# Kernel optimization log

Hardware: AMD Instinct MI355X
Metric: run time of the kernel (lower is better)

Reference implementation:

```python
import jax, jax.numpy as jnp
import numpy as np

D_MODEL, HEAD_DIM = 1024, 128

def setup_inputs() -> dict:
    key = jax.random.key(0)
    kx, kq, kk, kv = jax.random.split(key, 4)
    x = jax.random.normal(kx, (4, 4096, D_MODEL), dtype=jnp.float32)
    s = 1.0 / np.sqrt(D_MODEL)
    Wq = jax.random.normal(kq, (D_MODEL, HEAD_DIM), dtype=jnp.float32) * s
    Wk = jax.random.normal(kk, (D_MODEL, HEAD_DIM), dtype=jnp.float32) * s
    Wv = jax.random.normal(kv, (D_MODEL, HEAD_DIM), dtype=jnp.float32) * s
    return {"x": x, "Wq": Wq, "Wk": Wk, "Wv": Wv}

def reference(x, Wq, Wk, Wv):
    # x: [b, s, d_model]; Wq/Wk/Wv: [d_model, head_dim]
    q = jnp.einsum('bsd,dh->bsh', x, Wq)
    k = jnp.einsum('bsd,dh->bsh', x, Wk)
    v = jnp.einsum('bsd,dh->bsh', x, Wv)
    seq = x.shape[1]
    scale = 1.0 / jnp.sqrt(jnp.asarray(q.shape[-1], q.dtype))
    scores = jnp.einsum('bqh,bkh->bqk', q, k) * scale  # [b, s, s]
    causal = jnp.tril(jnp.ones((seq, seq), dtype=bool))
    scores = jnp.where(causal, scores, jnp.asarray(-jnp.inf, scores.dtype))
    attn = jax.nn.softmax(scores, axis=-1)
    return jnp.einsum('bqk,bkh->bqh', attn, v)
```

## Files before the change

### kernel.cpp

```cpp
#include <hip/hip_runtime.h>
#include <hip/hip_bf16.h>
#include <math.h>

#define D_MODEL 1024
#define HD 128
#define SEQ 4096

typedef __bf16 bf16x8 __attribute__((ext_vector_type(8)));
typedef float f32x4 __attribute__((ext_vector_type(4)));
typedef unsigned int u32;
typedef u32 u32x4 __attribute__((ext_vector_type(4)));

__device__ __forceinline__ unsigned short f2bf(float f) {
    union { float f; u32 u; } c; c.f = f;
    u32 u = c.u;
    u = (u + 0x7fffu + ((u >> 16) & 1u)) >> 16;
    return (unsigned short)u;
}
__device__ __forceinline__ u32 pk2(float a, float b) {
    __hip_bfloat162 h = __float22bfloat162_rn(make_float2(a, b));
    union { __hip_bfloat162 h; u32 u; } c; c.h = h; return c.u;
}

__global__ __launch_bounds__(256)
void wt_kernel(const float* __restrict__ Wq, const float* __restrict__ Wk,
               const float* __restrict__ Wv, unsigned short* __restrict__ Wt) {
    __shared__ float wsf[64][129];
    const int t = threadIdx.x;
    const int k0 = blockIdx.x * 64;
    const int mat = blockIdx.y;
    const float* W = (mat == 0) ? Wq : (mat == 1) ? Wk : Wv;
    const float sc = (mat == 0) ? (0.08838834764831845f * 1.4426950408889634f) : 1.0f;
    {
        const int r = t >> 2, c = (t & 3) * 32;
        const float* src = W + (size_t)(k0 + r) * HD + c;
        #pragma unroll
        for (int j = 0; j < 32; j += 4)
            *reinterpret_cast<f32x4*>(&wsf[r][c + j]) = *reinterpret_cast<const f32x4*>(src + j);
    }
    __syncthreads();
    const int n = t >> 1, ks = (t & 1) * 32;
    u32 ow[16];
    #pragma unroll
    for (int j = 0; j < 16; ++j)
        ow[j] = pk2(wsf[ks + 2 * j][n] * sc, wsf[ks + 2 * j + 1][n] * sc);
    unsigned short* dst = Wt + (size_t)(mat * HD + n) * D_MODEL + k0 + ks;
    #pragma unroll
    for (int j = 0; j < 4; ++j)
        *reinterpret_cast<u32x4*>(dst + j * 8) = (u32x4){ow[4*j], ow[4*j+1], ow[4*j+2], ow[4*j+3]};
}

__global__ __launch_bounds__(256)
void proj_kernel(const float* __restrict__ x, const unsigned short* __restrict__ Wt,
                 unsigned short* __restrict__ Qb, unsigned short* __restrict__ Kb,
                 unsigned short* __restrict__ Vt) {
    __shared__ __align__(16) unsigned short xs[64][72];
    __shared__ __align__(16) unsigned short wts[128][72];
    const int t = threadIdx.x;
    const int w = t >> 6, lane = t & 63, li = lane & 15, g2 = lane >> 4;
    const int nbase = blockIdx.x * 128;
    const int rowbase = blockIdx.y * 64;
    const int xr = t >> 2, xc = (t & 3) * 16;
    const int wr = t >> 1, wc = (t & 1) * 32;

    f32x4 acc[8];
    #pragma unroll
    for (int nt = 0; nt < 8; ++nt) acc[nt] = (f32x4){0.f, 0.f, 0.f, 0.f};

    f32x4 xv[4];
    bf16x8 wv[4];
    {
        const float* xp = x + (size_t)(rowbase + xr) * D_MODEL + xc;
        #pragma unroll
        for (int j = 0; j < 4; ++j) xv[j] = *reinterpret_cast<const f32x4*>(xp + j * 4);
        const unsigned short* wp = Wt + (size_t)(nbase + wr) * D_MODEL + wc;
        #pragma unroll
        for (int j = 0; j < 4; ++j) wv[j] = *reinterpret_cast<const bf16x8*>(wp + j * 8);
    }

    for (int k0 = 0; k0 < D_MODEL; k0 += 64) {
        union { u32 d[8]; bf16x8 v[2]; } cv;
        cv.d[0] = pk2(xv[0][0], xv[0][1]); cv.d[1] = pk2(xv[0][2], xv[0][3]);
        cv.d[2] = pk2(xv[1][0], xv[1][1]); cv.d[3] = pk2(xv[1][2], xv[1][3]);
        cv.d[4] = pk2(xv[2][0], xv[2][1]); cv.d[5] = pk2(xv[2][2], xv[2][3]);
        cv.d[6] = pk2(xv[3][0], xv[3][1]); cv.d[7] = pk2(xv[3][2], xv[3][3]);
        *reinterpret_cast<bf16x8*>(&xs[xr][xc])     = cv.v[0];
        *reinterpret_cast<bf16x8*>(&xs[xr][xc + 8]) = cv.v[1];
        #pragma unroll
        for (int j = 0; j < 4; ++j)
            *reinterpret_cast<bf16x8*>(&wts[wr][wc + j * 8]) = wv[j];
        __syncthreads();
        if (k0 + 64 < D_MODEL) {
            const float* xp = x + (size_t)(rowbase + xr) * D_MODEL + (k0 + 64) + xc;
            #pragma unroll
            for (int j = 0; j < 4; ++j) xv[j] = *reinterpret_cast<const f32x4*>(xp + j * 4);
            const unsigned short* wp = Wt + (size_t)(nbase + wr) * D_MODEL + (k0 + 64) + wc;
            #pragma unroll
            for (int j = 0; j < 4; ++j) wv[j] = *reinterpret_cast<const bf16x8*>(wp + j * 8);
        }
        #pragma unroll
        for (int kk = 0; kk < 2; ++kk) {
            bf16x8 af = *reinterpret_cast<const bf16x8*>(&xs[w * 16 + li][kk * 32 + g2 * 8]);
            #pragma unroll
            for (int nt = 0; nt < 8; ++nt) {
                bf16x8 bfr = *reinterpret_cast<const bf16x8*>(&wts[nt * 16 + li][kk * 32 + g2 * 8]);
                acc[nt] = __builtin_amdgcn_mfma_f32_16x16x32_bf16(af, bfr, acc[nt], 0, 0, 0);
            }
        }
        __syncthreads();
    }

    if (nbase < 256) {
        unsigned short* P = nbase ? Kb : Qb;
        #pragma unroll
        for (int nt = 0; nt < 8; ++nt)
            #pragma unroll
            for (int r = 0; r < 4; ++r) {
                int grow = rowbase + w * 16 + g2 * 4 + r;
                P[(size_t)grow * HD + nt * 16 + li] = f2bf(acc[nt][r]);
            }
    } else {
        int grow0 = rowbase + w * 16 + g2 * 4;
        int b_ = grow0 >> 12, s_ = grow0 & 4095;
        #pragma unroll
        for (int nt = 0; nt < 8; ++nt) {
            ushort4 s4;
            s4.x = f2bf(acc[nt][0]); s4.y = f2bf(acc[nt][1]);
            s4.z = f2bf(acc[nt][2]); s4.w = f2bf(acc[nt][3]);
            *reinterpret_cast<ushort4*>(&Vt[((size_t)b_ * HD + nt * 16 + li) * SEQ + s_]) = s4;
        }
    }
}

__global__ __launch_bounds__(256, 2)
void attn_kernel(const unsigned short* __restrict__ Qb, const unsigned short* __restrict__ Kb,
                 const unsigned short* __restrict__ Vt, float* __restrict__ outO,
                 unsigned short* __restrict__ Obf, float* __restrict__ Lbuf) {
    __shared__ __align__(16) char smem[46080];
    unsigned short (*Klds)[136] = (unsigned short(*)[136])(smem);
    unsigned short (*Vlds)[72]  = (unsigned short(*)[72])(smem + 17408);
    const int t = threadIdx.x;
    const int w = t >> 6, lane = t & 63, li = lane & 15, g2 = lane >> 4;
    const int qh = w >> 1, kh = w & 1;
    unsigned short (*Pw)[40] = (unsigned short(*)[40])(smem + 35840 + w * 2560);

    const int b = blockIdx.x & 3;
    const int u = blockIdx.x >> 2;
    const int g = 63 - (u >> 2);
    const int c = u & 3;
    const int R = g + 1;
    const int ts = (c * R) >> 2, te = ((c + 1) * R) >> 2;
    const int q0 = g * 64;
    const size_t rowb = (size_t)b * SEQ;
    const int koff = kh * 32;

    const int kr = t >> 2, kc = (t & 3) * 32;
    const int vr = t >> 1, vc = (t & 1) * 32;

    bf16x8 qf[2][4];
    #pragma unroll
    for (int qt = 0; qt < 2; ++qt)
        #pragma unroll
        for (int ks = 0; ks < 4; ++ks)
            qf[qt][ks] = *reinterpret_cast<const bf16x8*>(
                Qb + (rowb + q0 + qh * 32 + qt * 16 + li) * HD + ks * 32 + g2 * 8);

    f32x4 acco[2][8];
    #pragma unroll
    for (int qt = 0; qt < 2; ++qt)
        #pragma unroll
        for (int dt = 0; dt < 8; ++dt) acco[qt][dt] = (f32x4){0.f, 0.f, 0.f, 0.f};
    float ls[2][4] = {{0.f,0.f,0.f,0.f},{0.f,0.f,0.f,0.f}};

    bf16x8 kv_[4], vv_[4];
    if (ts < te) {
        const unsigned short* kp = Kb + (rowb + (size_t)ts * 64 + kr) * HD + kc;
        const unsigned short* vp = Vt + ((size_t)b * HD + vr) * SEQ + (size_t)ts * 64 + vc;
        #pragma unroll
        for (int j = 0; j < 4; ++j) kv_[j] = *reinterpret_cast<const bf16x8*>(kp + j * 8);
        #pragma unroll
        for (int j = 0; j < 4; ++j) vv_[j] = *reinterpret_cast<const bf16x8*>(vp + j * 8);
    }

    for (int it = ts; it < te; ++it) {
        #pragma unroll
        for (int j = 0; j < 4; ++j)
            *reinterpret_cast<bf16x8*>(&Klds[kr][kc + j * 8]) = kv_[j];
        #pragma unroll
        for (int j = 0; j < 4; ++j)
            *reinterpret_cast<bf16x8*>(&Vlds[vr][vc + j * 8]) = vv_[j];
        __syncthreads();
        if (it + 1 < te) {
            const unsigned short* kp = Kb + (rowb + (size_t)(it + 1) * 64 + kr) * HD + kc;
            const unsigned short* vp = Vt + ((size_t)b * HD + vr) * SEQ + (size_t)(it + 1) * 64 + vc;
            #pragma unroll
            for (int j = 0; j < 4; ++j) kv_[j] = *reinterpret_cast<const bf16x8*>(kp + j * 8);
            #pragma unroll
            for (int j = 0; j < 4; ++j) vv_[j] = *reinterpret_cast<const bf16x8*>(vp + j * 8);
        }

        f32x4 accs[2][2];
        #pragma unroll
        for (int qt = 0; qt < 2; ++qt)
            #pragma unroll
            for (int kt = 0; kt < 2; ++kt) accs[qt][kt] = (f32x4){0.f, 0.f, 0.f, 0.f};
        #pragma unroll
        for (int kt = 0; kt < 2; ++kt)
            #pragma unroll
            for (int ks = 0; ks < 4; ++ks) {
                bf16x8 kf = *reinterpret_cast<const bf16x8*>(&Klds[koff + kt * 16 + li][ks * 32 + g2 * 8]);
                accs[0][kt] = __builtin_amdgcn_mfma_f32_16x16x32_bf16(qf[0][ks], kf, accs[0][kt], 0, 0, 0);
                accs[1][kt] = __builtin_amdgcn_mfma_f32_16x16x32_bf16(qf[1][ks], kf, accs[1][kt], 0, 0, 0);
            }

        const bool masked = (it == g);
        float p[2][2][4];
        #pragma unroll
        for (int qt = 0; qt < 2; ++qt)
            #pragma unroll
            for (int kt = 0; kt < 2; ++kt)
                #pragma unroll
                for (int r = 0; r < 4; ++r) {
                    float s = accs[qt][kt][r];
                    if (masked && (koff + kt * 16 + li > qh * 32 + qt * 16 + g2 * 4 + r))
                        s = -INFINITY;
                    p[qt][kt][r] = __builtin_amdgcn_exp2f(s - 16.0f);
                }
        #pragma unroll
        for (int qt = 0; qt < 2; ++qt)
            #pragma unroll
            for (int r = 0; r < 4; ++r)
                ls[qt][r] += p[qt][0][r] + p[qt][1][r];

        #pragma unroll
        for (int qt = 0; qt < 2; ++qt)
            #pragma unroll
            for (int kt = 0; kt < 2; ++kt)
                #pragma unroll
                for (int r = 0; r < 4; ++r)
                    Pw[qt * 16 + g2 * 4 + r][kt * 16 + li] = f2bf(p[qt][kt][r]);
        bf16x8 pf0 = *reinterpret_cast<const bf16x8*>(&Pw[li][g2 * 8]);
        bf16x8 pf1 = *reinterpret_cast<const bf16x8*>(&Pw[16 + li][g2 * 8]);

        #pragma unroll
        for (int dt = 0; dt < 8; ++dt) {
            bf16x8 vf = *reinterpret_cast<const bf16x8*>(&Vlds[dt * 16 + li][koff + g2 * 8]);
            acco[0][dt] = __builtin_amdgcn_mfma_f32_16x16x32_bf16(pf0, vf, acco[0][dt], 0, 0, 0);
            acco[1][dt] = __builtin_amdgcn_mfma_f32_16x16x32_bf16(pf1, vf, acco[1][dt], 0, 0, 0);
        }
        __syncthreads();
    }

    #pragma unroll
    for (int d = 1; d < 16; d <<= 1)
        #pragma unroll
        for (int qt = 0; qt < 2; ++qt)
            #pragma unroll
            for (int r = 0; r < 4; ++r)
                ls[qt][r] += __shfl_xor(ls[qt][r], d);

    float (*Osum)[132] = (float(*)[132])smem;
    float* Lsh = (float*)(smem + 33792);
    __syncthreads();
    if (kh == 0) {
        #pragma unroll
        for (int qt = 0; qt < 2; ++qt) {
            #pragma unroll
            for (int dt = 0; dt < 8; ++dt)
                #pragma unroll
                for (int r = 0; r < 4; ++r)
                    Osum[qh * 32 + qt * 16 + g2 * 4 + r][dt * 16 + li] = acco[qt][dt][r];
            if (li == 0)
                #pragma unroll
                for (int r = 0; r < 4; ++r)
                    Lsh[qh * 32 + qt * 16 + g2 * 4 + r] = ls[qt][r];
        }
    }
    __syncthreads();
    if (kh == 1) {
        #pragma unroll
        for (int qt = 0; qt < 2; ++qt) {
            #pragma unroll
            for (int dt = 0; dt < 8; ++dt)
                #pragma unroll
                for (int r = 0; r < 4; ++r)
                    Osum[qh * 32 + qt * 16 + g2 * 4 + r][dt * 16 + li] += acco[qt][dt][r];
            if (li == 0)
                #pragma unroll
                for (int r = 0; r < 4; ++r)
                    Lsh[64 + qh * 32 + qt * 16 + g2 * 4 + r] = ls[qt][r];
        }
    }
    __syncthreads();

    if (t < 64)
        Lbuf[(size_t)c * 16384 + rowb + q0 + t] = Lsh[t] + Lsh[64 + t];
    #pragma unroll
    for (int k = 0; k < 8; ++k) {
        int idx = t + k * 256;
        int row = idx >> 5, col = (idx & 31) * 4;
        f32x4 o = *reinterpret_cast<const f32x4*>(&Osum[row][col]);
        size_t grow = rowb + q0 + row;
        if (c == 3) {
            *reinterpret_cast<f32x4*>(&outO[grow * HD + col]) = o;
        } else {
            u32 lo = pk2(o[0], o[1]), hi = pk2(o[2], o[3]);
            union { u32 d[2]; uint2 v; } pkd; pkd.d[0] = lo; pkd.d[1] = hi;
            *reinterpret_cast<uint2*>(&Obf[(size_t)c * 2097152 + grow * HD + col]) = pkd.v;
        }
    }
}

__global__ __launch_bounds__(256)
void merge_kernel(float* __restrict__ outO, const unsigned short* __restrict__ Obf,
                  const float* __restrict__ Lbuf) {
    int tid = blockIdx.x * 256 + threadIdx.x;
    #pragma unroll
    for (int k = 0; k < 4; ++k) {
        int idx = tid + k * 131072;
        int row = idx >> 5, col = (idx & 31) * 4;
        float l = Lbuf[row] + Lbuf[16384 + row] + Lbuf[32768 + row] + Lbuf[49152 + row];
        float inv = 1.f / l;
        f32x4 o = *reinterpret_cast<const f32x4*>(&outO[(size_t)row * HD + col]);
        #pragma unroll
        for (int c = 0; c < 3; ++c) {
            ushort4 u = *reinterpret_cast<const ushort4*>(&Obf[(size_t)c * 2097152 + (size_t)row * HD + col]);
            union { u32 u; float f; } a, b2, c2, d2;
            a.u = (u32)u.x << 16; b2.u = (u32)u.y << 16;
            c2.u = (u32)u.z << 16; d2.u = (u32)u.w << 16;
            o[0] += a.f; o[1] += b2.f; o[2] += c2.f; o[3] += d2.f;
        }
        #pragma unroll
        for (int j = 0; j < 4; ++j) o[j] *= inv;
        *reinterpret_cast<f32x4*>(&outO[(size_t)row * HD + col]) = o;
    }
}

extern "C" void kernel_launch(void* const* d_in, const int* in_sizes, int n_in,
                              void* d_out, int out_size, void* d_ws, size_t ws_size,
                              hipStream_t stream) {
    const float* x  = (const float*)d_in[0];
    const float* Wq = (const float*)d_in[1];
    const float* Wk = (const float*)d_in[2];
    const float* Wv = (const float*)d_in[3];
    float* out = (float*)d_out;

    char* ws = (char*)d_ws;
    unsigned short* Qb  = (unsigned short*)(ws);
    unsigned short* Kb  = (unsigned short*)(ws + ((size_t)4  << 20));
    unsigned short* Vt  = (unsigned short*)(ws + ((size_t)8  << 20));
    unsigned short* Wt  = (unsigned short*)(ws + ((size_t)12 << 20));
    unsigned short* Obf = (unsigned short*)(ws + ((size_t)13 << 20));
    float*          Lb  = (float*)(ws + ((size_t)25 << 20));

    wt_kernel   <<<dim3(16, 3),  dim3(256), 0, stream>>>(Wq, Wk, Wv, Wt);
    proj_kernel <<<dim3(3, 256), dim3(256), 0, stream>>>(x, Wt, Qb, Kb, Vt);
    attn_kernel <<<dim3(1024),   dim3(256), 0, stream>>>(Qb, Kb, Vt, out, Obf, Lb);
    merge_kernel<<<dim3(512),    dim3(256), 0, stream>>>(out, Obf, Lb);
}
```

Before: 177.6 us.

## Use direct global-to-LDS DMA with XOR swizzled layouts in projection and attention

Both the projection and attention kernels now use global_load_lds to copy tiles straight into shared memory, replacing register-staged copies. The LDS tiles use XOR-swizzled layouts instead of padding, which avoids bank conflicts while shrinking shared memory. The projection kernel double-buffers 32-wide k-steps and converts x to bf16 after reading it from LDS. The attention kernel lowers its LDS footprint and raises launch bounds to 4 blocks per CU for more occupancy, at the risk of register pressure and an exposed load latency, since its next-tile DMA is issued only after the trailing barrier.

```diff
diff --git a/kernel.cpp b/kernel.cpp
--- a/kernel.cpp
+++ b/kernel.cpp
@@ -20,6 +20,11 @@
 __device__ __forceinline__ u32 pk2(float a, float b) {
     __hip_bfloat162 h = __float22bfloat162_rn(make_float2(a, b));
     union { __hip_bfloat162 h; u32 u; } c; c.h = h; return c.u;
+}
+__device__ __forceinline__ void dma16(void* lds, const void* g) {
+    __builtin_amdgcn_global_load_lds(
+        (const __attribute__((address_space(1))) u32*)g,
+        (__attribute__((address_space(3))) u32*)lds, 16, 0, 0);
 }
 
 __global__ __launch_bounds__(256)
@@ -54,60 +59,52 @@
 void proj_kernel(const float* __restrict__ x, const unsigned short* __restrict__ Wt,
                  unsigned short* __restrict__ Qb, unsigned short* __restrict__ Kb,
                  unsigned short* __restrict__ Vt) {
-    __shared__ __align__(16) unsigned short xs[64][72];
-    __shared__ __align__(16) unsigned short wts[128][72];
+    __shared__ __align__(1024) char ps[32768];
     const int t = threadIdx.x;
-    const int w = t >> 6, lane = t & 63, li = lane & 15, g2 = lane >> 4;
+    const int w = t >> 6, l = t & 63, li = l & 15, g2 = l >> 4;
     const int nbase = blockIdx.x * 128;
     const int rowbase = blockIdx.y * 64;
-    const int xr = t >> 2, xc = (t & 3) * 16;
-    const int wr = t >> 1, wc = (t & 1) * 32;
 
     f32x4 acc[8];
     #pragma unroll
     for (int nt = 0; nt < 8; ++nt) acc[nt] = (f32x4){0.f, 0.f, 0.f, 0.f};
 
-    f32x4 xv[4];
-    bf16x8 wv[4];
-    {
-        const float* xp = x + (size_t)(rowbase + xr) * D_MODEL + xc;
-        #pragma unroll
-        for (int j = 0; j < 4; ++j) xv[j] = *reinterpret_cast<const f32x4*>(xp + j * 4);
-        const unsigned short* wp = Wt + (size_t)(nbase + wr) * D_MODEL + wc;
-        #pragma unroll
-        for (int j = 0; j < 4; ++j) wv[j] = *reinterpret_cast<const bf16x8*>(wp + j * 8);
-    }
-
-    for (int k0 = 0; k0 < D_MODEL; k0 += 64) {
-        union { u32 d[8]; bf16x8 v[2]; } cv;
-        cv.d[0] = pk2(xv[0][0], xv[0][1]); cv.d[1] = pk2(xv[0][2], xv[0][3]);
-        cv.d[2] = pk2(xv[1][0], xv[1][1]); cv.d[3] = pk2(xv[1][2], xv[1][3]);
-        cv.d[4] = pk2(xv[2][0], xv[2][1]); cv.d[5] = pk2(xv[2][2], xv[2][3]);
-        cv.d[6] = pk2(xv[3][0], xv[3][1]); cv.d[7] = pk2(xv[3][2], xv[3][3]);
-        *reinterpret_cast<bf16x8*>(&xs[xr][xc])     = cv.v[0];
-        *reinterpret_cast<bf16x8*>(&xs[xr][xc + 8]) = cv.v[1];
-        #pragma unroll
-        for (int j = 0; j < 4; ++j)
-            *reinterpret_cast<bf16x8*>(&wts[wr][wc + j * 8]) = wv[j];
+    const int lrow = l >> 3;
+    const int xg = (l & 7) ^ (lrow & 6);
+    const int wgr = (l & 7) ^ lrow;
+    const int wrow_add = (wgr >> 2) << 6;
+    const int wkc = (wgr & 3) * 8;
+
+    auto stage = [&](int k0, int buf) {
+        #pragma unroll
+        for (int j = 0; j < 2; ++j) {
+            int r0 = w * 16 + 8 * j;
+            dma16(ps + buf * 8192 + r0 * 128,
+                  x + (size_t)(rowbase + r0 + lrow) * D_MODEL + k0 + xg * 4);
+            dma16(ps + 16384 + buf * 8192 + r0 * 128,
+                  Wt + (size_t)(nbase + r0 + lrow + wrow_add) * D_MODEL + k0 + wkc);
+        }
+    };
+
+    stage(0, 0);
+    for (int it = 0; it < 32; ++it) {
+        const int buf = it & 1;
         __syncthreads();
-        if (k0 + 64 < D_MODEL) {
-            const float* xp = x + (size_t)(rowbase + xr) * D_MODEL + (k0 + 64) + xc;
-            #pragma unroll
-            for (int j = 0; j < 4; ++j) xv[j] = *reinterpret_cast<const f32x4*>(xp + j * 4);
-            const unsigned short* wp = Wt + (size_t)(nbase + wr) * D_MODEL + (k0 + 64) + wc;
-            #pragma unroll
-            for (int j = 0; j < 4; ++j) wv[j] = *reinterpret_cast<const bf16x8*>(wp + j * 8);
-        }
-        #pragma unroll
-        for (int kk = 0; kk < 2; ++kk) {
-            bf16x8 af = *reinterpret_cast<const bf16x8*>(&xs[w * 16 + li][kk * 32 + g2 * 8]);
-            #pragma unroll
-            for (int nt = 0; nt < 8; ++nt) {
-                bf16x8 bfr = *reinterpret_cast<const bf16x8*>(&wts[nt * 16 + li][kk * 32 + g2 * 8]);
-                acc[nt] = __builtin_amdgcn_mfma_f32_16x16x32_bf16(af, bfr, acc[nt], 0, 0, 0);
-            }
-        }
-        __syncthreads();
+        if (it + 1 < 32) stage((it + 1) * 32, buf ^ 1);
+        const char* xb = ps + buf * 8192 + (w * 16 + li) * 128 + (((2 * g2) ^ (li & 6)) * 16);
+        f32x4 x0 = *reinterpret_cast<const f32x4*>(xb);
+        f32x4 x1 = *reinterpret_cast<const f32x4*>(xb + 16);
+        union { u32 d[4]; bf16x8 v; } cva;
+        cva.d[0] = pk2(x0[0], x0[1]); cva.d[1] = pk2(x0[2], x0[3]);
+        cva.d[2] = pk2(x1[0], x1[1]); cva.d[3] = pk2(x1[2], x1[3]);
+        bf16x8 af = cva.v;
+        #pragma unroll
+        for (int nt = 0; nt < 8; ++nt) {
+            bf16x8 bfr = *reinterpret_cast<const bf16x8*>(
+                ps + 16384 + buf * 8192 + ((nt & 3) * 16 + li) * 128 +
+                ((((nt >> 2) * 4 + g2) ^ (li & 7)) * 16));
+            acc[nt] = __builtin_amdgcn_mfma_f32_16x16x32_bf16(af, bfr, acc[nt], 0, 0, 0);
+        }
     }
 
     if (nbase < 256) {
@@ -132,18 +129,14 @@
     }
 }
 
-__global__ __launch_bounds__(256, 2)
+__global__ __launch_bounds__(256, 4)
 void attn_kernel(const unsigned short* __restrict__ Qb, const unsigned short* __restrict__ Kb,
                  const unsigned short* __restrict__ Vt, float* __restrict__ outO,
                  unsigned short* __restrict__ Obf, float* __restrict__ Lbuf) {
-    __shared__ __align__(16) char smem[46080];
-    unsigned short (*Klds)[136] = (unsigned short(*)[136])(smem);
-    unsigned short (*Vlds)[72]  = (unsigned short(*)[72])(smem + 17408);
+    __shared__ __align__(1024) char smem[40960];
     const int t = threadIdx.x;
-    const int w = t >> 6, lane = t & 63, li = lane & 15, g2 = lane >> 4;
+    const int w = t >> 6, l = t & 63, li = l & 15, g2 = l >> 4;
     const int qh = w >> 1, kh = w & 1;
-    unsigned short (*Pw)[40] = (unsigned short(*)[40])(smem + 35840 + w * 2560);
-
     const int b = blockIdx.x & 3;
     const int u = blockIdx.x >> 2;
     const int g = 63 - (u >> 2);
@@ -154,8 +147,22 @@
     const size_t rowb = (size_t)b * SEQ;
     const int koff = kh * 32;
 
-    const int kr = t >> 2, kc = (t & 3) * 32;
-    const int vr = t >> 1, vc = (t & 1) * 32;
+    const unsigned short* KbB = Kb + rowb * HD;
+    const unsigned short* VtB = Vt + (size_t)b * HD * SEQ;
+    const int vgran = ((l & 7) ^ (l >> 3)) * 8;
+
+    auto stage = [&](int it) {
+        const int j0 = it * 64;
+        #pragma unroll
+        for (int j = 0; j < 4; ++j) {
+            int rK = w * 16 + 4 * j + (l >> 4);
+            dma16(smem + (w * 16 + 4 * j) * 256,
+                  KbB + (size_t)(j0 + rK) * 128 + (((l & 15) ^ (rK & 7)) * 8));
+            int rV = w * 32 + 8 * j + (l >> 3);
+            dma16(smem + 16384 + (w * 32 + 8 * j) * 128,
+                  VtB + (size_t)rV * SEQ + j0 + vgran);
+        }
+    };
 
     bf16x8 qf[2][4];
     #pragma unroll
@@ -172,32 +179,11 @@
         for (int dt = 0; dt < 8; ++dt) acco[qt][dt] = (f32x4){0.f, 0.f, 0.f, 0.f};
     float ls[2][4] = {{0.f,0.f,0.f,0.f},{0.f,0.f,0.f,0.f}};
 
-    bf16x8 kv_[4], vv_[4];
-    if (ts < te) {
-        const unsigned short* kp = Kb + (rowb + (size_t)ts * 64 + kr) * HD + kc;
-        const unsigned short* vp = Vt + ((size_t)b * HD + vr) * SEQ + (size_t)ts * 64 + vc;
-        #pragma unroll
-        for (int j = 0; j < 4; ++j) kv_[j] = *reinterpret_cast<const bf16x8*>(kp + j * 8);
-        #pragma unroll
-        for (int j = 0; j < 4; ++j) vv_[j] = *reinterpret_cast<const bf16x8*>(vp + j * 8);
-    }
-
+    const int gV = ((4 * kh + g2) ^ (li & 7)) * 16;
+
+    if (ts < te) stage(ts);
     for (int it = ts; it < te; ++it) {
-        #pragma unroll
-        for (int j = 0; j < 4; ++j)
-            *reinterpret_cast<bf16x8*>(&Klds[kr][kc + j * 8]) = kv_[j];
-        #pragma unroll
-        for (int j = 0; j < 4; ++j)
-            *reinterpret_cast<bf16x8*>(&Vlds[vr][vc + j * 8]) = vv_[j];
         __syncthreads();
-        if (it + 1 < te) {
-            const unsigned short* kp = Kb + (rowb + (size_t)(it + 1) * 64 + kr) * HD + kc;
-            const unsigned short* vp = Vt + ((size_t)b * HD + vr) * SEQ + (size_t)(it + 1) * 64 + vc;
-            #pragma unroll
-            for (int j = 0; j < 4; ++j) kv_[j] = *reinterpret_cast<const bf16x8*>(kp + j * 8);
-            #pragma unroll
-            for (int j = 0; j < 4; ++j) vv_[j] = *reinterpret_cast<const bf16x8*>(vp + j * 8);
-        }
 
         f32x4 accs[2][2];
         #pragma unroll
@@ -205,16 +191,17 @@
             #pragma unroll
             for (int kt = 0; kt < 2; ++kt) accs[qt][kt] = (f32x4){0.f, 0.f, 0.f, 0.f};
         #pragma unroll
-        for (int kt = 0; kt < 2; ++kt)
+        for (int kt = 0; kt < 2; ++kt) {
+            const char* kb = smem + (koff + kt * 16 + li) * 256;
             #pragma unroll
             for (int ks = 0; ks < 4; ++ks) {
-                bf16x8 kf = *reinterpret_cast<const bf16x8*>(&Klds[koff + kt * 16 + li][ks * 32 + g2 * 8]);
+                bf16x8 kf = *reinterpret_cast<const bf16x8*>(kb + (((4 * ks + g2) ^ (li & 7)) * 16));
                 accs[0][kt] = __builtin_amdgcn_mfma_f32_16x16x32_bf16(qf[0][ks], kf, accs[0][kt], 0, 0, 0);
                 accs[1][kt] = __builtin_amdgcn_mfma_f32_16x16x32_bf16(qf[1][ks], kf, accs[1][kt], 0, 0, 0);
             }
+        }
 
         const bool masked = (it == g);
-        float p[2][2][4];
         #pragma unroll
         for (int qt = 0; qt < 2; ++qt)
             #pragma unroll
@@ -224,31 +211,24 @@
                     float s = accs[qt][kt][r];
                     if (masked && (koff + kt * 16 + li > qh * 32 + qt * 16 + g2 * 4 + r))
                         s = -INFINITY;
-                    p[qt][kt][r] = __builtin_amdgcn_exp2f(s - 16.0f);
+                    float p = __builtin_amdgcn_exp2f(s - 16.0f);
+                    ls[qt][r] += p;
+                    int prow = qh * 32 + qt * 16 + g2 * 4 + r;
+                    int gw = (4 * kh + 2 * kt + (li >> 3)) ^ ((4 * g2 + r) & 7);
+                    *reinterpret_cast<unsigned short*>(
+                        smem + 32768 + prow * 128 + gw * 16 + (li & 7) * 2) = f2bf(p);
                 }
-        #pragma unroll
-        for (int qt = 0; qt < 2; ++qt)
-            #pragma unroll
-            for (int r = 0; r < 4; ++r)
-                ls[qt][r] += p[qt][0][r] + p[qt][1][r];
-
-        #pragma unroll
-        for (int qt = 0; qt < 2; ++qt)
-            #pragma unroll
-            for (int kt = 0; kt < 2; ++kt)
-                #pragma unroll
-                for (int r = 0; r < 4; ++r)
-                    Pw[qt * 16 + g2 * 4 + r][kt * 16 + li] = f2bf(p[qt][kt][r]);
-        bf16x8 pf0 = *reinterpret_cast<const bf16x8*>(&Pw[li][g2 * 8]);
-        bf16x8 pf1 = *reinterpret_cast<const bf16x8*>(&Pw[16 + li][g2 * 8]);
-
+
+        bf16x8 pf0 = *reinterpret_cast<const bf16x8*>(smem + 32768 + (qh * 32 + li) * 128 + gV);
+        bf16x8 pf1 = *reinterpret_cast<const bf16x8*>(smem + 32768 + (qh * 32 + 16 + li) * 128 + gV);
         #pragma unroll
         for (int dt = 0; dt < 8; ++dt) {
-            bf16x8 vf = *reinterpret_cast<const bf16x8*>(&Vlds[dt * 16 + li][koff + g2 * 8]);
+            bf16x8 vf = *reinterpret_cast<const bf16x8*>(smem + 16384 + (dt * 16 + li) * 128 + gV);
             acco[0][dt] = __builtin_amdgcn_mfma_f32_16x16x32_bf16(pf0, vf, acco[0][dt], 0, 0, 0);
             acco[1][dt] = __builtin_amdgcn_mfma_f32_16x16x32_bf16(pf1, vf, acco[1][dt], 0, 0, 0);
         }
         __syncthreads();
+        if (it + 1 < te) stage(it + 1);
     }
 
     #pragma unroll
@@ -304,8 +284,8 @@
         if (c == 3) {
             *reinterpret_cast<f32x4*>(&outO[grow * HD + col]) = o;
         } else {
-            u32 lo = pk2(o[0], o[1]), hi = pk2(o[2], o[3]);
-            union { u32 d[2]; uint2 v; } pkd; pkd.d[0] = lo; pkd.d[1] = hi;
+            union { u32 d[2]; uint2 v; } pkd;
+            pkd.d[0] = pk2(o[0], o[1]); pkd.d[1] = pk2(o[2], o[3]);
             *reinterpret_cast<uint2*>(&Obf[(size_t)c * 2097152 + grow * HD + col]) = pkd.v;
         }
     }
@@ -319,15 +299,16 @@
     for (int k = 0; k < 4; ++k) {
         int idx = tid + k * 131072;
         int row = idx >> 5, col = (idx & 31) * 4;
-        float l = Lbuf[row] + Lbuf[16384 + row] + Lbuf[32768 + row] + Lbuf[49152 + row];
-        float inv = 1.f / l;
+        float lsum = Lbuf[row] + Lbuf[16384 + row] + Lbuf[32768 + row] + Lbuf[49152 + row];
+        float inv = 1.f / lsum;
         f32x4 o = *reinterpret_cast<const f32x4*>(&outO[(size_t)row * HD + col]);
         #pragma unroll
-        for (int c = 0; c < 3; ++c) {
-            ushort4 u = *reinterpret_cast<const ushort4*>(&Obf[(size_t)c * 2097152 + (size_t)row * HD + col]);
+        for (int cc = 0; cc < 3; ++cc) {
+            ushort4 uu = *reinterpret_cast<const ushort4*>(
+                &Obf[(size_t)cc * 2097152 + (size_t)row * HD + col]);
             union { u32 u; float f; } a, b2, c2, d2;
-            a.u = (u32)u.x << 16; b2.u = (u32)u.y << 16;
-            c2.u = (u32)u.z << 16; d2.u = (u32)u.w << 16;
+            a.u = (u32)uu.x << 16; b2.u = (u32)uu.y << 16;
+            c2.u = (u32)uu.z << 16; d2.u = (u32)uu.w << 16;
             o[0] += a.f; o[1] += b2.f; o[2] += c2.f; o[3] += d2.f;
         }
         #pragma unroll
```

New measurement: 258.8 us. +45.7%, slower.
